# Performance work log

Hardware: AMD Instinct MI355X
Metric: run time of the kernel (lower is better)

The kernel has to match this reference:

```python
import jax, jax.numpy as jnp
import numpy as np

B, C_IN, T, F = 8, 64, 128, 32
MAIN, AUX = 128, 64
D_IN, N_ST, DT_R = 256, 16, 8  # Mamba: d_inner=2*128, d_state=16, dt_rank=ceil(128/16)
SQ2 = 0.70710678
BN_S = 1.0 / np.sqrt(1.0 + 1e-5)  # eval BN with running stats (0,1)


def silu(x):
    return x * jax.nn.sigmoid(x)


def bn2d(x, g, b):
    return x * (g * BN_S)[None, :, None, None] + b[None, :, None, None]


def dwconv(x, w, b, pad):
    y = jax.lax.conv_general_dilated(
        x, w, (1, 1), ((pad, pad), (pad, pad)),
        dimension_numbers=('NCHW', 'OIHW', 'NCHW'),
        feature_group_count=x.shape[1])
    return y + b[None, :, None, None]


def mamba(x, in_w, conv_w, conv_b, xproj_w, dt_w, dt_b, A_log, D, out_w):
    # x: [B, L, d_model]
    Bsz, L, _ = x.shape
    xz = x @ in_w.T                       # [B,L,2*D_IN]
    xi, z = xz[..., :D_IN], xz[..., D_IN:]
    # causal depthwise conv1d, d_conv=4
    xp = jnp.pad(xi, ((0, 0), (3, 0), (0, 0)))
    xc = sum(xp[:, k:k + L, :] * conv_w[:, k] for k in range(4)) + conv_b
    xc = silu(xc)                          # [B,L,D_IN]
    x_dbl = xc @ xproj_w.T                 # [B,L,DT_R+2N]
    dt = jax.nn.softplus(x_dbl[..., :DT_R] @ dt_w.T + dt_b)   # [B,L,D_IN]
    Bt = x_dbl[..., DT_R:DT_R + N_ST]      # [B,L,N]
    Ct = x_dbl[..., DT_R + N_ST:]          # [B,L,N]
    A = -jnp.exp(A_log)                    # [D_IN,N]

    def step(h, inp):
        d_t, B_t, C_t, x_t = inp           # [B,D_IN],[B,N],[B,N],[B,D_IN]
        h = jnp.exp(d_t[..., None] * A) * h + (d_t * x_t)[..., None] * B_t[:, None, :]
        return h, jnp.einsum('bdn,bn->bd', h, C_t)

    h0 = jnp.zeros((Bsz, D_IN, N_ST), x.dtype)
    _, ys = jax.lax.scan(step, h0, (dt.transpose(1, 0, 2), Bt.transpose(1, 0, 2),
                                    Ct.transpose(1, 0, 2), xc.transpose(1, 0, 2)))
    y = ys.transpose(1, 0, 2) + D * xc
    return (y * silu(z)) @ out_w.T


def patch_proj(z, w, b, g, beta):
    bz, c, t2, f = z.shape
    zr = z.reshape(bz, c, t2, f // 2, 2)
    y = jnp.einsum('bctfp,ocp->botf', zr, w) + b[None, :, None, None]
    return jax.nn.relu(bn2d(y, g, beta))


def setup_inputs() -> dict:
    keys = iter(jax.random.split(jax.random.key(0), 64))

    def rn(shape, s=0.1):
        return jax.random.normal(next(keys), shape, jnp.float32) * s

    Alog = jnp.tile(jnp.log(jnp.arange(1, N_ST + 1, dtype=jnp.float32)), (D_IN, 1))
    d = {
        'x': rn((B, C_IN, T, F), 1.0),
        'main_w': rn((MAIN, C_IN, 2)), 'main_b': rn((MAIN,)),
        'main_g': jnp.ones((MAIN,)), 'main_beta': jnp.zeros((MAIN,)),
        'aux_w': rn((AUX, C_IN, 2)), 'aux_b': rn((AUX,)),
        'aux_g': jnp.ones((AUX,)), 'aux_beta': jnp.zeros((AUX,)),
        'ln_g': jnp.ones((MAIN,)), 'ln_b': jnp.zeros((MAIN,)),
        'vim_w': rn((MAIN, MAIN), 0.05), 'vim_b': jnp.zeros((MAIN,)),
        'mk3_w': rn((32, 1, 3, 3)), 'mk3_b': rn((32,)),
        'mk5_w': rn((32, 1, 5, 5)), 'mk5_b': rn((32,)),
        'mk_g': jnp.ones((AUX,)), 'mk_beta': jnp.zeros((AUX,)),
        'fus_w': rn((192, 192), 0.05), 'fus_b': jnp.zeros((192,)),
        'fus_g': jnp.ones((192,)), 'fus_beta': jnp.zeros((192,)),
        'rec_w': rn((192, C_IN, 2, 2), 0.05), 'rec_b': jnp.zeros((C_IN,)),
        'rec_g': jnp.ones((C_IN,)), 'rec_beta': jnp.zeros((C_IN,)),
    }
    for p in ('f', 'b'):
        d[p + '_in_w'] = rn((2 * D_IN, MAIN), 0.05)
        d[p + '_conv_w'] = rn((D_IN, 4))
        d[p + '_conv_b'] = rn((D_IN,))
        d[p + '_xproj_w'] = rn((DT_R + 2 * N_ST, D_IN), 0.05)
        d[p + '_dt_w'] = rn((D_IN, DT_R))
        d[p + '_dt_b'] = rn((D_IN,))
        d[p + '_Alog'] = Alog
        d[p + '_D'] = jnp.ones((D_IN,))
        d[p + '_out_w'] = rn((MAIN, D_IN), 0.05)
    return d


def reference(x, main_w, main_b, main_g, main_beta, aux_w, aux_b, aux_g, aux_beta,
              ln_g, ln_b,
              f_in_w, f_conv_w, f_conv_b, f_xproj_w, f_dt_w, f_dt_b, f_Alog, f_D, f_out_w,
              b_in_w, b_conv_w, b_conv_b, b_xproj_w, b_dt_w, b_dt_b, b_Alog, b_D, b_out_w,
              vim_w, vim_b, mk3_w, mk3_b, mk5_w, mk5_b, mk_g, mk_beta,
              fus_w, fus_b, fus_g, fus_beta, rec_w, rec_b, rec_g, rec_beta):
    # Haar wavelet along time (stride 2)
    xe, xo = x[:, :, 0::2, :], x[:, :, 1::2, :]
    low = (xe + xo) * SQ2
    high = (xo - xe) * SQ2                  # [B,C,T/2,F]
    main_in = patch_proj(low, main_w, main_b, main_g, main_beta)   # [B,128,T/2,F/2]
    aux_in = patch_proj(high, aux_w, aux_b, aux_g, aux_beta)       # [B,64,T/2,F/2]

    bz, c, h, w = main_in.shape
    x_seq = main_in.reshape(bz, c, h * w).transpose(0, 2, 1)       # [B,L,128]
    # VimBlock: LayerNorm -> bidirectional Mamba -> out_proj + residual
    mu = x_seq.mean(-1, keepdims=True)
    var = ((x_seq - mu) ** 2).mean(-1, keepdims=True)
    xn = (x_seq - mu) / jnp.sqrt(var + 1e-5) * ln_g + ln_b
    of = mamba(xn, f_in_w, f_conv_w, f_conv_b, f_xproj_w, f_dt_w, f_dt_b, f_Alog, f_D, f_out_w)
    ob = mamba(xn[:, ::-1, :], b_in_w, b_conv_w, b_conv_b, b_xproj_w, b_dt_w, b_dt_b,
               b_Alog, b_D, b_out_w)[:, ::-1, :]
    x_main_seq = (of + ob) @ vim_w.T + vim_b + x_seq
    x_main = x_main_seq.transpose(0, 2, 1).reshape(bz, c, h, w)

    # multi-kernel depthwise branch
    a1 = dwconv(aux_in[:, :32], mk3_w, mk3_b, 1)
    a2 = dwconv(aux_in[:, 32:], mk5_w, mk5_b, 2)
    x_aux = silu(bn2d(jnp.concatenate([a1, a2], axis=1), mk_g, mk_beta))

    x_in = jnp.concatenate([main_in, aux_in], axis=1)
    x_out = jnp.concatenate([x_main, x_aux], axis=1)
    fus = jnp.einsum('bcij,oc->boij', x_out, fus_w) + fus_b[None, :, None, None]
    x_fused = x_in + bn2d(fus, fus_g, fus_beta)

    # ConvTranspose2d kernel=stride=2 (non-overlapping) -> einsum + interleave reshape
    y = jnp.einsum('bcij,cokl->boikjl', x_fused, rec_w)
    y = y.reshape(bz, rec_w.shape[1], h * 2, w * 2) + rec_b[None, :, None, None]
    y = jax.nn.relu(bn2d(y, rec_g, rec_beta))
    return y + x
```

## Files before the change

### kernel.cpp

```cpp
#include <hip/hip_runtime.h>
#include <hip/hip_bf16.h>

#define SQ2F 0.70710678f
#define BNS 0.9999950000374997f
#define L_ 1024
#define TS 32
#define SEGL 128
#define WARM 64

typedef __attribute__((ext_vector_type(8))) short bf16x8;
typedef __attribute__((ext_vector_type(8))) unsigned short us8;
typedef __attribute__((ext_vector_type(4))) float f32x4;

__device__ __forceinline__ float silu_f(float v) { return v / (1.f + __expf(-v)); }
__device__ __forceinline__ unsigned short f2b(float f) {
    unsigned u = __float_as_uint(f);
    return (unsigned short)((u + 0x7FFFu + ((u >> 16) & 1u)) >> 16);
}

#define AR_XPC0 155648
#define AR_XPC1 229376
#define AR_END  471040

__global__ __launch_bounds__(256) void sentinel_sE(float* out, int n) {
    int i = blockIdx.x * 256 + threadIdx.x;
    if (i < n) out[i] = 1.0e6f;
}

__global__ __launch_bounds__(256) void wavelet_sE(const float* x, float* low, float* high, int b0) {
    int idx = blockIdx.x * 256 + threadIdx.x;
    int fq = idx & 31, i = (idx >> 5) & 63, c = (idx >> 11) & 63, bl = idx >> 17;
    size_t base = ((size_t)((b0 + bl) * 64 + c) * 128 + 2 * i) * 32 + fq;
    float xe = x[base];
    float xo = x[base + 32];
    int m = (bl * 64 + i) * 16 + (fq >> 1);
    int k = c * 2 + (fq & 1);
    low[(size_t)m * 128 + k]  = (xe + xo) * SQ2F;
    high[(size_t)m * 128 + k] = (xo - xe) * SQ2F;
}

__global__ __launch_bounds__(256) void wcvt_sE(
    const float* main_w, const float* aux_w, const float* in_w0, const float* in_w1,
    const float* xp0, const float* xp1, const float* vim_w, const float* fus_w,
    const float* ow0, const float* ow1, const float* rec_w, unsigned short* dst) {
    int i = blockIdx.x * 256 + threadIdx.x;
    float v;
    if      (i < 16384)  v = main_w[i];
    else if (i < 24576)  v = aux_w[i - 16384];
    else if (i < 90112)  v = in_w0[i - 24576];
    else if (i < 155648) v = in_w1[i - 90112];
    else if (i < 163840) { int j = i - 155648; v = xp0[(size_t)((j >> 8) + 8) * 256 + (j & 255)]; }
    else if (i < 229376) return;
    else if (i < 237568) { int j = i - 229376; v = xp1[(size_t)((j >> 8) + 8) * 256 + (j & 255)]; }
    else if (i < 303104) return;
    else if (i < 319488) v = vim_w[i - 303104];
    else if (i < 356352) v = fus_w[i - 319488];
    else if (i < 421888) {
        int j = i - 356352; int k = j & 511; int n = j >> 9;
        v = (k < 256) ? ow0[(size_t)n * 256 + k] : ow1[(size_t)n * 256 + (k - 256)];
    } else if (i < AR_END) {
        int j = i - 421888; int n = j / 192, c = j % 192;
        v = rec_w[((size_t)(c * 64 + (n >> 2)) * 2 + ((n >> 1) & 1)) * 2 + (n & 1)];
    } else return;
    dst[i] = f2b(v);
}

__global__ __launch_bounds__(256) void wcomp_sE(const float* xp0, const float* xp1,
                                                const float* dtw0, const float* dtw1,
                                                unsigned short* arena) {
    int idx = blockIdx.x * 256 + threadIdx.x;
    int dir = blockIdx.y;
    int d = idx >> 8, k = idx & 255;
    const float* xp = dir ? xp1 : xp0;
    const float* dtw = dir ? dtw1 : dtw0;
    float v = 0.f;
#pragma unroll
    for (int r = 0; r < 8; ++r) v = fmaf(dtw[d * 8 + r], xp[(size_t)r * 256 + k], v);
    arena[(size_t)(dir ? AR_XPC1 : AR_XPC0) + (size_t)(32 + d) * 256 + k] = f2b(v);
}

__global__ __launch_bounds__(256) void mgemm_sE(
    const float* A, const float* A2, const unsigned short* W, float* C,
    int N, int K, int lda, int ldw, int ldc,
    int aflip, int cflip, int adual, int epi, int b0g, int agate,
    const float* bias, const float* gg, const float* bet,
    const float* xm, const float* xa, const float* xres, float* outf,
    const float* A1, const unsigned short* W1, float* C1, int N1, int aflip1,
    const float* bias1, const float* gg1, const float* bet1, float* outf1) {
    if (blockIdx.z) {
        A = A1; W = W1; C = C1; N = N1; aflip = aflip1;
        bias = bias1; gg = gg1; bet = bet1; outf = outf1;
    }
    __shared__ unsigned short Ab[2][4][128][8];
    __shared__ unsigned short Wl[2][4][64][8];
    const int tid = threadIdx.x;
    const int wave = tid >> 6, lane = tid & 63;
    const int m0 = blockIdx.x * 128;
    const int n0 = blockIdx.y * 64;

    const int rA = tid >> 1, hA = tid & 1;
    const int nS = tid >> 2, gS = tid & 3;
    int m_a = m0 + rA;
    if (aflip) m_a ^= 1023;
    const float* Arow = A + (size_t)m_a * lda;
    const float* A2row = adual ? (A2 + (size_t)((m0 + rA) ^ 1023) * lda - 256) : Arow;
    const bool wok = (n0 + nS) < N;
    const unsigned short* Wrow = W + (size_t)(n0 + nS) * ldw;

    f32x4 acc[2][4];
#pragma unroll
    for (int i = 0; i < 2; ++i)
#pragma unroll
        for (int j = 0; j < 4; ++j) acc[i][j] = f32x4{0.f, 0.f, 0.f, 0.f};

    const int nk = K >> 5;
    float4 v0, v1, v2, v3;
    us8 wv;

    auto loadregs = [&](int kt) {
        const int k0 = kt * 32 + hA * 16;
        const float* src = (adual && k0 >= 256) ? A2row : Arow;
        v0 = *(const float4*)(src + k0);
        v1 = *(const float4*)(src + k0 + 4);
        v2 = *(const float4*)(src + k0 + 8);
        v3 = *(const float4*)(src + k0 + 12);
        if (agate) {
            float4 g0 = *(const float4*)(src + k0 + 256);
            float4 g1 = *(const float4*)(src + k0 + 260);
            float4 g2 = *(const float4*)(src + k0 + 264);
            float4 g3 = *(const float4*)(src + k0 + 268);
            v0.x *= silu_f(g0.x); v0.y *= silu_f(g0.y); v0.z *= silu_f(g0.z); v0.w *= silu_f(g0.w);
            v1.x *= silu_f(g1.x); v1.y *= silu_f(g1.y); v1.z *= silu_f(g1.z); v1.w *= silu_f(g1.w);
            v2.x *= silu_f(g2.x); v2.y *= silu_f(g2.y); v2.z *= silu_f(g2.z); v2.w *= silu_f(g2.w);
            v3.x *= silu_f(g3.x); v3.y *= silu_f(g3.y); v3.z *= silu_f(g3.z); v3.w *= silu_f(g3.w);
        }
        if (wok) wv = *(const us8*)(Wrow + kt * 32 + gS * 8);
        else     wv = us8{0, 0, 0, 0, 0, 0, 0, 0};
    };
    auto writelds = [&](int buf) {
        us8 lo, hi;
        lo[0] = f2b(v0.x); lo[1] = f2b(v0.y); lo[2] = f2b(v0.z); lo[3] = f2b(v0.w);
        lo[4] = f2b(v1.x); lo[5] = f2b(v1.y); lo[6] = f2b(v1.z); lo[7] = f2b(v1.w);
        hi[0] = f2b(v2.x); hi[1] = f2b(v2.y); hi[2] = f2b(v2.z); hi[3] = f2b(v2.w);
        hi[4] = f2b(v3.x); hi[5] = f2b(v3.y); hi[6] = f2b(v3.z); hi[7] = f2b(v3.w);
        *(us8*)&Ab[buf][2 * hA][rA][0] = lo;
        *(us8*)&Ab[buf][2 * hA + 1][rA][0] = hi;
        *(us8*)&Wl[buf][gS][nS][0] = wv;
    };

    loadregs(0);
    writelds(0);
    __syncthreads();

    const int li = lane & 15, kg = lane >> 4;
    for (int t = 0; t < nk; ++t) {
        if (t + 1 < nk) loadregs(t + 1);
        const int cb = t & 1;
        bf16x8 af0 = *(const bf16x8*)&Ab[cb][kg][wave * 32 + li][0];
        bf16x8 af1 = *(const bf16x8*)&Ab[cb][kg][wave * 32 + 16 + li][0];
        bf16x8 wf0 = *(const bf16x8*)&Wl[cb][kg][li][0];
        bf16x8 wf1 = *(const bf16x8*)&Wl[cb][kg][16 + li][0];
        bf16x8 wf2 = *(const bf16x8*)&Wl[cb][kg][32 + li][0];
        bf16x8 wf3 = *(const bf16x8*)&Wl[cb][kg][48 + li][0];
        acc[0][0] = __builtin_amdgcn_mfma_f32_16x16x32_bf16(af0, wf0, acc[0][0], 0, 0, 0);
        acc[0][1] = __builtin_amdgcn_mfma_f32_16x16x32_bf16(af0, wf1, acc[0][1], 0, 0, 0);
        acc[0][2] = __builtin_amdgcn_mfma_f32_16x16x32_bf16(af0, wf2, acc[0][2], 0, 0, 0);
        acc[0][3] = __builtin_amdgcn_mfma_f32_16x16x32_bf16(af0, wf3, acc[0][3], 0, 0, 0);
        acc[1][0] = __builtin_amdgcn_mfma_f32_16x16x32_bf16(af1, wf0, acc[1][0], 0, 0, 0);
        acc[1][1] = __builtin_amdgcn_mfma_f32_16x16x32_bf16(af1, wf1, acc[1][1], 0, 0, 0);
        acc[1][2] = __builtin_amdgcn_mfma_f32_16x16x32_bf16(af1, wf2, acc[1][2], 0, 0, 0);
        acc[1][3] = __builtin_amdgcn_mfma_f32_16x16x32_bf16(af1, wf3, acc[1][3], 0, 0, 0);
        if (t + 1 < nk) writelds((t + 1) & 1);
        __syncthreads();
    }

#pragma unroll
    for (int mf = 0; mf < 2; ++mf) {
#pragma unroll
        for (int nf = 0; nf < 4; ++nf) {
#pragma unroll
            for (int rr = 0; rr < 4; ++rr) {
                int m = m0 + wave * 32 + mf * 16 + (lane >> 4) * 4 + rr;
                int n = n0 + nf * 16 + (lane & 15);
                if (n >= N) continue;
                float v = acc[mf][nf][rr];
                int bb = m >> 10, l = m & 1023;
                if (epi == 0) {
                    int mm = cflip ? (m ^ 1023) : m;
                    C[(size_t)mm * ldc + n] = v;
                } else if (epi == 1) {
                    v += bias[n];
                    v = v * (gg[n] * BNS) + bet[n];
                    C[((size_t)(bb * N + n) << 10) + l] = fmaxf(v, 0.f);
                } else if (epi == 2) {
                    C[(size_t)m * ldc + n] = v + bias[n] + xm[((size_t)(bb * 128 + n) << 10) + l];
                } else if (epi == 3) {
                    float xin = (n < 128) ? xm[((size_t)(bb * 128 + n) << 10) + l]
                                          : xa[((size_t)(bb * 64 + (n - 128)) << 10) + l];
                    C[(size_t)m * ldc + n] = xin + (v + bias[n]) * (gg[n] * BNS) + bet[n];
                } else if (epi == 4) {
                    int o = n >> 2, kq = (n >> 1) & 1, l2 = n & 1;
                    int ii = l >> 4, jj = l & 15;
                    v += bias[o];
                    v = fmaxf(v * (gg[o] * BNS) + bet[o], 0.f);
                    size_t oidx = ((size_t)((b0g + bb) * 64 + o) * 128 + (2 * ii + kq)) * 32 + (2 * jj + l2);
                    outf[oidx] = v + xres[oidx];
                } else {
                    if (n < 32) {
                        C[(size_t)m * 32 + n] = v;
                    } else {
                        float a = v + bias[n - 32];
                        float sp = (a > 15.f) ? a : __logf(1.f + __expf(a));
                        outf[(size_t)m * 256 + (n - 32)] = sp;
                    }
                }
            }
        }
    }
}

__global__ __launch_bounds__(256) void ln_sE(const float* mainin, const float* g,
                                             const float* bt, float* xn) {
    __shared__ float tile[128][65];
    __shared__ float red0[4][64];
    __shared__ float red1[4][64];
    __shared__ float mu_s[64];
    __shared__ float rs_s[64];
    const int bb = blockIdx.y;
    const int l0 = blockIdx.x * 64;
    const int tid = threadIdx.x;
    for (int idx = tid; idx < 128 * 64; idx += 256) {
        int c = idx >> 6, l = idx & 63;
        tile[c][l] = mainin[((size_t)(bb * 128 + c) << 10) + l0 + l];
    }
    __syncthreads();
    {
        int l = tid & 63, q = tid >> 6;
        float s = 0.f, s2 = 0.f;
#pragma unroll
        for (int c0 = 0; c0 < 32; ++c0) {
            float v = tile[q * 32 + c0][l];
            s += v; s2 = fmaf(v, v, s2);
        }
        red0[q][l] = s; red1[q][l] = s2;
    }
    __syncthreads();
    if (tid < 64) {
        float S = red0[0][tid] + red0[1][tid] + red0[2][tid] + red0[3][tid];
        float S2 = red1[0][tid] + red1[1][tid] + red1[2][tid] + red1[3][tid];
        float mu = S * (1.f / 128.f);
        float var = S2 * (1.f / 128.f) - mu * mu;
        mu_s[tid] = mu;
        rs_s[tid] = rsqrtf(var + 1e-5f);
    }
    __syncthreads();
    for (int idx = tid; idx < 128 * 64; idx += 256) {
        int l = idx >> 7, c = idx & 127;
        float v = (tile[c][l] - mu_s[l]) * rs_s[l] * g[c] + bt[c];
        xn[((size_t)(bb << 10) + l0 + l) * 128 + c] = v;
    }
}

__global__ __launch_bounds__(256) void conv_sE(const float* xzf, const float* xzb,
                                               const float* cw0, const float* cb0,
                                               const float* cw1, const float* cb1,
                                               float* xcf, float* xcb2) {
    int m = blockIdx.x, d = threadIdx.x, dir = blockIdx.y;
    const float* xz = dir ? xzb : xzf;
    const float* cw = dir ? cw1 : cw0;
    const float* cb = dir ? cb1 : cb0;
    float* xc = dir ? xcb2 : xcf;
    int l = m & 1023;
    float acc = cb[d];
    const float* w = cw + d * 4;
    for (int k = 0; k < 4; ++k) {
        int ls = l - 3 + k;
        if (ls >= 0) acc = fmaf(xz[(size_t)(m - 3 + k) * 512 + d], w[k], acc);
    }
    xc[(size_t)m * 256 + d] = silu_f(acc);
}

#define STAGE_SE(L0V, SBV)                                                                  \
    {                                                                                       \
        const int l0_ = (L0V), sb_ = (SBV);                                                 \
        _Pragma("unroll")                                                                   \
        for (int f = t2; f < TS * 4; f += 64) {                                             \
            int l = f >> 2, sg = (f & 3) * 4;                                               \
            *(float4*)&xvs[sb_][l][sg] = *(const float4*)(xcb + base256 + (size_t)(l0_ + l) * 256 + sg); \
            *(float4*)&dts[sb_][l][sg] = *(const float4*)(dlb + base256 + (size_t)(l0_ + l) * 256 + sg); \
        }                                                                                   \
        _Pragma("unroll")                                                                   \
        for (int f = t2; f < TS * 8; f += 64) {                                             \
            int l = f >> 3, sg = (f & 7) * 4;                                               \
            *(float4*)&bcs[sb_][l][sg] = *(const float4*)(xdb + base32 + (size_t)(l0_ + l) * 32 + sg);   \
        }                                                                                   \
    }

__global__ __launch_bounds__(128) void scan_sE(
    const float* xc0, const float* xc1, const float* dtl0, const float* dtl1,
    const float* xd0, const float* xd1,
    const float* al0, const float* al1, const float* D0, const float* D1,
    float* y0, float* y1) {
    __shared__ float dts[2][TS][16];
    __shared__ float xvs[2][TS][16];
    __shared__ float bcs[2][TS][32];

    const int b = blockIdx.x;
    const int dir = blockIdx.y;
    const int seg = blockIdx.z >> 4;
    const int d0 = (blockIdx.z & 15) * 16;
    const int tid = threadIdx.x;

    const float* xcb = dir ? xc1 : xc0;
    const float* dlb = dir ? dtl1 : dtl0;
    const float* xdb = dir ? xd1 : xd0;
    float* ygb = dir ? y1 : y0;

    const size_t base256 = (size_t)b * L_ * 256 + d0;
    const size_t base32  = (size_t)b * L_ * 32;

    const int lstart = seg * SEGL - (seg ? WARM : 0);
    const int ntiles = (seg ? (SEGL + WARM) : SEGL) / TS;
    const int wtiles = seg ? (WARM / TS) : 0;

    const int isStage = tid >> 6;
    const int t2 = tid & 63;
    const int dg = t2 >> 2, q = t2 & 3;

    const float LOG2E = 1.44269504088896340736f;
    float al2[4];
    float Dd = 0.f;
    float h0 = 0.f, h1 = 0.f, h2 = 0.f, h3 = 0.f;
    if (!isStage) {
        const float* alog = (dir ? al1 : al0) + (d0 + dg) * 16 + q * 4;
#pragma unroll
        for (int n = 0; n < 4; ++n) al2[n] = -__expf(alog[n]) * LOG2E;
        Dd = (dir ? D1 : D0)[d0 + dg];
    }
    float* yp = ygb + (size_t)b * L_ * 512 + d0 + dg;

    if (isStage) STAGE_SE(lstart, 0);
    __syncthreads();

    for (int t = 0; t < ntiles; ++t) {
        if (isStage) {
            if (t + 1 < ntiles) STAGE_SE(lstart + (t + 1) * TS, (t + 1) & 1);
        } else {
            const int cb = t & 1;
            const bool dostore = (t >= wtiles);
#pragma unroll 4
            for (int l = 0; l < TS; ++l) {
                float dt = dts[cb][l][dg];
                float xv = xvs[cb][l][dg];
                float4 Bv = *(const float4*)&bcs[cb][l][q * 4];
                float4 Cv = *(const float4*)&bcs[cb][l][16 + q * 4];
                float dtx = dt * xv;
                float e0 = exp2f(dt * al2[0]);
                float e1 = exp2f(dt * al2[1]);
                float e2 = exp2f(dt * al2[2]);
                float e3 = exp2f(dt * al2[3]);
                h0 = fmaf(e0, h0, dtx * Bv.x);
                h1 = fmaf(e1, h1, dtx * Bv.y);
                h2 = fmaf(e2, h2, dtx * Bv.z);
                h3 = fmaf(e3, h3, dtx * Bv.w);
                float acc = fmaf(h3, Cv.w, fmaf(h2, Cv.z, fmaf(h1, Cv.y, h0 * Cv.x)));
                acc += __shfl_xor(acc, 1);
                acc += __shfl_xor(acc, 2);
                if (dostore && q == 0) {
                    yp[(size_t)(lstart + t * TS + l) * 512] = fmaf(Dd, xv, acc);
                }
            }
        }
        __syncthreads();
    }
}

__global__ __launch_bounds__(256) void dwconv_sE(const float* auxin,
                                                 const float* mk3w, const float* mk3b,
                                                 const float* mk5w, const float* mk5b,
                                                 const float* mkg, const float* mkbeta,
                                                 float* xout) {
    int idx = blockIdx.x * 256 + threadIdx.x;
    int j = idx & 15, i = (idx >> 4) & 63, c = (idx >> 10) & 63, b = idx >> 16;
    const float* src = auxin + ((size_t)(b * 64 + c) << 10);
    float acc;
    if (c < 32) {
        acc = mk3b[c];
        for (int di = -1; di <= 1; ++di)
            for (int dj = -1; dj <= 1; ++dj) {
                int ii = i + di, jj = j + dj;
                if (ii >= 0 && ii < 64 && jj >= 0 && jj < 16)
                    acc = fmaf(src[ii * 16 + jj], mk3w[(c * 3 + di + 1) * 3 + dj + 1], acc);
            }
    } else {
        int cc = c - 32;
        acc = mk5b[cc];
        for (int di = -2; di <= 2; ++di)
            for (int dj = -2; dj <= 2; ++dj) {
                int ii = i + di, jj = j + dj;
                if (ii >= 0 && ii < 64 && jj >= 0 && jj < 16)
                    acc = fmaf(src[ii * 16 + jj], mk5w[(cc * 5 + di + 2) * 5 + dj + 2], acc);
            }
    }
    float v = acc * (mkg[c] * BNS) + mkbeta[c];
    v = silu_f(v);
    xout[(size_t)((b << 10) + i * 16 + j) * 192 + 128 + c] = v;
}

extern "C" void kernel_launch(void* const* d_in, const int* in_sizes, int n_in,
                              void* d_out, int out_size, void* d_ws, size_t ws_size,
                              hipStream_t stream) {
    (void)in_sizes; (void)n_in;
    const float* X         = (const float*)d_in[0];
    const float* main_w    = (const float*)d_in[1];
    const float* main_b    = (const float*)d_in[2];
    const float* main_g    = (const float*)d_in[3];
    const float* main_beta = (const float*)d_in[4];
    const float* aux_w     = (const float*)d_in[5];
    const float* aux_b     = (const float*)d_in[6];
    const float* aux_g     = (const float*)d_in[7];
    const float* aux_beta  = (const float*)d_in[8];
    const float* ln_g      = (const float*)d_in[9];
    const float* ln_b      = (const float*)d_in[10];
    const float* vim_w     = (const float*)d_in[11];
    const float* vim_b     = (const float*)d_in[12];
    const float* mk3_w     = (const float*)d_in[13];
    const float* mk3_b     = (const float*)d_in[14];
    const float* mk5_w     = (const float*)d_in[15];
    const float* mk5_b     = (const float*)d_in[16];
    const float* mk_g      = (const float*)d_in[17];
    const float* mk_beta   = (const float*)d_in[18];
    const float* fus_w     = (const float*)d_in[19];
    const float* fus_b     = (const float*)d_in[20];
    const float* fus_g     = (const float*)d_in[21];
    const float* fus_beta  = (const float*)d_in[22];
    const float* rec_w     = (const float*)d_in[23];
    const float* rec_b     = (const float*)d_in[24];
    const float* rec_g     = (const float*)d_in[25];
    const float* rec_beta  = (const float*)d_in[26];
    const float* in_w0    = (const float*)d_in[27];
    const float* conv_w0  = (const float*)d_in[28];
    const float* conv_b0  = (const float*)d_in[29];
    const float* xproj_w0 = (const float*)d_in[30];
    const float* dt_w0    = (const float*)d_in[31];
    const float* dt_b0    = (const float*)d_in[32];
    const float* Alog0    = (const float*)d_in[33];
    const float* Dvec0    = (const float*)d_in[34];
    const float* out_w0   = (const float*)d_in[35];
    const float* in_w1    = (const float*)d_in[36];
    const float* conv_w1  = (const float*)d_in[37];
    const float* conv_b1  = (const float*)d_in[38];
    const float* xproj_w1 = (const float*)d_in[39];
    const float* dt_w1    = (const float*)d_in[40];
    const float* dt_b1    = (const float*)d_in[41];
    const float* Alog1    = (const float*)d_in[42];
    const float* Dvec1    = (const float*)d_in[43];
    const float* out_w1   = (const float*)d_in[44];

    const size_t wf = ws_size / sizeof(float);
    const size_t FIX = AR_END / 2;
    int nb = 0;
    if      (FIX + (size_t)8 * 1024 * 2432 <= wf) nb = 8;
    else if (FIX + (size_t)4 * 1024 * 2432 <= wf) nb = 4;
    else if (FIX + (size_t)2 * 1024 * 2432 <= wf) nb = 2;
    else if (FIX + (size_t)1 * 1024 * 2432 <= wf) nb = 1;
    if (nb == 0) {
        sentinel_sE<<<(out_size + 255) / 256, 256, 0, stream>>>((float*)d_out, out_size);
        return;
    }

    float* ws = (float*)d_ws;
    unsigned short* warena = (unsigned short*)ws;
    const unsigned short* bmain = warena;
    const unsigned short* baux  = warena + 16384;
    const unsigned short* bin0  = warena + 24576;
    const unsigned short* bin1  = warena + 90112;
    const unsigned short* bxpc0 = warena + AR_XPC0;
    const unsigned short* bxpc1 = warena + AR_XPC1;
    const unsigned short* bvim  = warena + 303104;
    const unsigned short* bfus  = warena + 319488;
    const unsigned short* bwcat = warena + 356352;
    const unsigned short* brec  = warena + 421888;

    const size_t R = (size_t)nb * 1024;
    float* xzf    = ws + FIX;
    float* xzb    = xzf + R * 512;
    float* mainin = xzb + R * 512;
    float* auxin  = mainin + R * 128;
    float* xn     = auxin + R * 64;
    float* vimin  = xn;
    float* lowb   = xn + R * 128;
    float* highb  = lowb + R * 128;
    float* dtlf   = lowb;
    float* xcf    = highb + R * 128;
    float* xcb    = xcf + R * 256;
    float* xoutc  = xcf;
    float* xfused = xcb;
    float* xdblf  = xcb + R * 256;
    float* xdblb  = xdblf + R * 32;
    float* dtlb   = xdblb + R * 32;

    wcvt_sE<<<1840, 256, 0, stream>>>(main_w, aux_w, in_w0, in_w1, xproj_w0, xproj_w1,
                                      vim_w, fus_w, out_w0, out_w1, rec_w, warena);
    wcomp_sE<<<dim3(256, 2), 256, 0, stream>>>(xproj_w0, xproj_w1, dt_w0, dt_w1, warena);
    const unsigned GM = (unsigned)(R / 128);

    for (int b0 = 0; b0 < 8; b0 += nb) {
        wavelet_sE<<<nb * 512, 256, 0, stream>>>(X, lowb, highb, b0);

        mgemm_sE<<<dim3(GM, 2, 2), 256, 0, stream>>>(
            lowb, nullptr, bmain, mainin, 128, 128, 128, 128, 0, 0, 0, 0, 1, 0, 0,
            main_b, main_g, main_beta, nullptr, nullptr, nullptr, nullptr,
            highb, baux, auxin, 64, 0, aux_b, aux_g, aux_beta, nullptr);
        ln_sE<<<dim3(16, nb), 256, 0, stream>>>(mainin, ln_g, ln_b, xn);

        mgemm_sE<<<dim3(GM, 8, 2), 256, 0, stream>>>(
            xn, nullptr, bin0, xzf, 512, 128, 128, 128, 512, 0, 0, 0, 0, 0, 0,
            nullptr, nullptr, nullptr, nullptr, nullptr, nullptr, nullptr,
            xn, bin1, xzb, 512, 1, nullptr, nullptr, nullptr, nullptr);

        conv_sE<<<dim3((unsigned)R, 2), 256, 0, stream>>>(
            xzf, xzb, conv_w0, conv_b0, conv_w1, conv_b1, xcf, xcb);

        mgemm_sE<<<dim3(GM, 5, 2), 256, 0, stream>>>(
            xcf, nullptr, bxpc0, xdblf, 288, 256, 256, 256, 32, 0, 0, 0, 5, 0, 0,
            dt_b0, nullptr, nullptr, nullptr, nullptr, nullptr, dtlf,
            xcb, bxpc1, xdblb, 288, 0, dt_b1, nullptr, nullptr, dtlb);

        scan_sE<<<dim3(nb, 2, 128), 128, 0, stream>>>(
            xcf, xcb, dtlf, dtlb, xdblf, xdblb,
            Alog0, Alog1, Dvec0, Dvec1, xzf, xzb);

        mgemm_sE<<<dim3(GM, 2, 1), 256, 0, stream>>>(
            xzf, xzb, bwcat, vimin, 128, 512, 512, 512, 128, 0, 0, 1, 0, 0, 1,
            nullptr, nullptr, nullptr, nullptr, nullptr, nullptr, nullptr,
            nullptr, nullptr, nullptr, 0, 0, nullptr, nullptr, nullptr, nullptr);

        mgemm_sE<<<dim3(GM, 2, 1), 256, 0, stream>>>(
            vimin, nullptr, bvim, xoutc, 128, 128, 128, 128, 192, 0, 0, 0, 2, 0, 0,
            vim_b, nullptr, nullptr, mainin, nullptr, nullptr, nullptr,
            nullptr, nullptr, nullptr, 0, 0, nullptr, nullptr, nullptr, nullptr);

        dwconv_sE<<<nb * 256, 256, 0, stream>>>(
            auxin, mk3_w, mk3_b, mk5_w, mk5_b, mk_g, mk_beta, xoutc);

        mgemm_sE<<<dim3(GM, 3, 1), 256, 0, stream>>>(
            xoutc, nullptr, bfus, xfused, 192, 192, 192, 192, 192, 0, 0, 0, 3, 0, 0,
            fus_b, fus_g, fus_beta, mainin, auxin, nullptr, nullptr,
            nullptr, nullptr, nullptr, 0, 0, nullptr, nullptr, nullptr, nullptr);

        mgemm_sE<<<dim3(GM, 4, 1), 256, 0, stream>>>(
            xfused, nullptr, brec, nullptr, 256, 192, 192, 192, 0, 0, 0, 0, 4, b0, 0,
            rec_b, rec_g, rec_beta, nullptr, nullptr, X, (float*)d_out,
            nullptr, nullptr, nullptr, 0, 0, nullptr, nullptr, nullptr, nullptr);
    }
}
```

Measured before the change: 241.6 us.

## Store Mamba intermediates in bf16 and halve scan segment length

Stores the layer-normed input, the in-projection output, the conv output, dt and the scan output as bf16 rather than fp32. The GEMM kernel gains flags to read bf16 A operands directly and write bf16 C. This roughly halves memory traffic between the Mamba stages and drops the per-tile fp32-to-bf16 conversion in the GEMM loads. The scan now uses 64-step segments with 32 warm-up steps, which doubles its grid for more parallelism but adds relative warm-up overhead and more approximation error in the state. The conv kernel handles two channels per thread with 128 threads.

```diff
diff --git a/kernel.cpp b/kernel.cpp
--- a/kernel.cpp
+++ b/kernel.cpp
@@ -5,29 +5,32 @@
 #define BNS 0.9999950000374997f
 #define L_ 1024
 #define TS 32
-#define SEGL 128
-#define WARM 64
+#define SEGL 64
+#define WARM 32
+#define NSEG 16
 
 typedef __attribute__((ext_vector_type(8))) short bf16x8;
 typedef __attribute__((ext_vector_type(8))) unsigned short us8;
 typedef __attribute__((ext_vector_type(4))) float f32x4;
+typedef unsigned short u16;
 
 __device__ __forceinline__ float silu_f(float v) { return v / (1.f + __expf(-v)); }
-__device__ __forceinline__ unsigned short f2b(float f) {
+__device__ __forceinline__ float u2f(u16 v) { return __uint_as_float(((unsigned)v) << 16); }
+__device__ __forceinline__ u16 f2b(float f) {
     unsigned u = __float_as_uint(f);
-    return (unsigned short)((u + 0x7FFFu + ((u >> 16) & 1u)) >> 16);
+    return (u16)((u + 0x7FFFu + ((u >> 16) & 1u)) >> 16);
 }
 
 #define AR_XPC0 155648
 #define AR_XPC1 229376
 #define AR_END  471040
 
-__global__ __launch_bounds__(256) void sentinel_sE(float* out, int n) {
+__global__ __launch_bounds__(256) void sentinel_sF(float* out, int n) {
     int i = blockIdx.x * 256 + threadIdx.x;
     if (i < n) out[i] = 1.0e6f;
 }
 
-__global__ __launch_bounds__(256) void wavelet_sE(const float* x, float* low, float* high, int b0) {
+__global__ __launch_bounds__(256) void wavelet_sF(const float* x, float* low, float* high, int b0) {
     int idx = blockIdx.x * 256 + threadIdx.x;
     int fq = idx & 31, i = (idx >> 5) & 63, c = (idx >> 11) & 63, bl = idx >> 17;
     size_t base = ((size_t)((b0 + bl) * 64 + c) * 128 + 2 * i) * 32 + fq;
@@ -39,10 +42,10 @@
     high[(size_t)m * 128 + k] = (xo - xe) * SQ2F;
 }
 
-__global__ __launch_bounds__(256) void wcvt_sE(
+__global__ __launch_bounds__(256) void wcvt_sF(
     const float* main_w, const float* aux_w, const float* in_w0, const float* in_w1,
     const float* xp0, const float* xp1, const float* vim_w, const float* fus_w,
-    const float* ow0, const float* ow1, const float* rec_w, unsigned short* dst) {
+    const float* ow0, const float* ow1, const float* rec_w, u16* dst) {
     int i = blockIdx.x * 256 + threadIdx.x;
     float v;
     if      (i < 16384)  v = main_w[i];
@@ -65,9 +68,9 @@
     dst[i] = f2b(v);
 }
 
-__global__ __launch_bounds__(256) void wcomp_sE(const float* xp0, const float* xp1,
+__global__ __launch_bounds__(256) void wcomp_sF(const float* xp0, const float* xp1,
                                                 const float* dtw0, const float* dtw1,
-                                                unsigned short* arena) {
+                                                u16* arena) {
     int idx = blockIdx.x * 256 + threadIdx.x;
     int dir = blockIdx.y;
     int d = idx >> 8, k = idx & 255;
@@ -79,20 +82,20 @@
     arena[(size_t)(dir ? AR_XPC1 : AR_XPC0) + (size_t)(32 + d) * 256 + k] = f2b(v);
 }
 
-__global__ __launch_bounds__(256) void mgemm_sE(
-    const float* A, const float* A2, const unsigned short* W, float* C,
+__global__ __launch_bounds__(256) void mgemm_sF(
+    const float* A, const float* A2, const u16* W, float* C,
     int N, int K, int lda, int ldw, int ldc,
-    int aflip, int cflip, int adual, int epi, int b0g, int agate,
+    int aflip, int cflip, int adual, int abf16, int cbf16, int epi, int b0g, int agate,
     const float* bias, const float* gg, const float* bet,
     const float* xm, const float* xa, const float* xres, float* outf,
-    const float* A1, const unsigned short* W1, float* C1, int N1, int aflip1,
+    const float* A1, const u16* W1, float* C1, int N1, int aflip1,
     const float* bias1, const float* gg1, const float* bet1, float* outf1) {
     if (blockIdx.z) {
         A = A1; W = W1; C = C1; N = N1; aflip = aflip1;
         bias = bias1; gg = gg1; bet = bet1; outf = outf1;
     }
-    __shared__ unsigned short Ab[2][4][128][8];
-    __shared__ unsigned short Wl[2][4][64][8];
+    __shared__ u16 Ab[2][4][128][8];
+    __shared__ u16 Wl[2][4][64][8];
     const int tid = threadIdx.x;
     const int wave = tid >> 6, lane = tid & 63;
     const int m0 = blockIdx.x * 128;
@@ -104,8 +107,10 @@
     if (aflip) m_a ^= 1023;
     const float* Arow = A + (size_t)m_a * lda;
     const float* A2row = adual ? (A2 + (size_t)((m0 + rA) ^ 1023) * lda - 256) : Arow;
+    const u16* ArowB = (const u16*)A + (size_t)m_a * lda;
+    const u16* A2rowB = adual ? ((const u16*)A2 + (size_t)((m0 + rA) ^ 1023) * lda - 256) : ArowB;
     const bool wok = (n0 + nS) < N;
-    const unsigned short* Wrow = W + (size_t)(n0 + nS) * ldw;
+    const u16* Wrow = W + (size_t)(n0 + nS) * ldw;
 
     f32x4 acc[2][4];
 #pragma unroll
@@ -115,34 +120,44 @@
 
     const int nk = K >> 5;
     float4 v0, v1, v2, v3;
+    us8 b0v, b1v;
     us8 wv;
 
     auto loadregs = [&](int kt) {
         const int k0 = kt * 32 + hA * 16;
-        const float* src = (adual && k0 >= 256) ? A2row : Arow;
-        v0 = *(const float4*)(src + k0);
-        v1 = *(const float4*)(src + k0 + 4);
-        v2 = *(const float4*)(src + k0 + 8);
-        v3 = *(const float4*)(src + k0 + 12);
-        if (agate) {
-            float4 g0 = *(const float4*)(src + k0 + 256);
-            float4 g1 = *(const float4*)(src + k0 + 260);
-            float4 g2 = *(const float4*)(src + k0 + 264);
-            float4 g3 = *(const float4*)(src + k0 + 268);
-            v0.x *= silu_f(g0.x); v0.y *= silu_f(g0.y); v0.z *= silu_f(g0.z); v0.w *= silu_f(g0.w);
-            v1.x *= silu_f(g1.x); v1.y *= silu_f(g1.y); v1.z *= silu_f(g1.z); v1.w *= silu_f(g1.w);
-            v2.x *= silu_f(g2.x); v2.y *= silu_f(g2.y); v2.z *= silu_f(g2.z); v2.w *= silu_f(g2.w);
-            v3.x *= silu_f(g3.x); v3.y *= silu_f(g3.y); v3.z *= silu_f(g3.z); v3.w *= silu_f(g3.w);
+        if (abf16) {
+            const u16* srcb = (adual && k0 >= 256) ? A2rowB : ArowB;
+            b0v = *(const us8*)(srcb + k0);
+            b1v = *(const us8*)(srcb + k0 + 8);
+            if (agate) {
+                us8 z0 = *(const us8*)(srcb + k0 + 256);
+                us8 z1 = *(const us8*)(srcb + k0 + 264);
+#pragma unroll
+                for (int i = 0; i < 8; ++i) {
+                    b0v[i] = f2b(u2f(b0v[i]) * silu_f(u2f(z0[i])));
+                    b1v[i] = f2b(u2f(b1v[i]) * silu_f(u2f(z1[i])));
+                }
+            }
+        } else {
+            const float* src = (adual && k0 >= 256) ? A2row : Arow;
+            v0 = *(const float4*)(src + k0);
+            v1 = *(const float4*)(src + k0 + 4);
+            v2 = *(const float4*)(src + k0 + 8);
+            v3 = *(const float4*)(src + k0 + 12);
         }
         if (wok) wv = *(const us8*)(Wrow + kt * 32 + gS * 8);
         else     wv = us8{0, 0, 0, 0, 0, 0, 0, 0};
     };
     auto writelds = [&](int buf) {
         us8 lo, hi;
-        lo[0] = f2b(v0.x); lo[1] = f2b(v0.y); lo[2] = f2b(v0.z); lo[3] = f2b(v0.w);
-        lo[4] = f2b(v1.x); lo[5] = f2b(v1.y); lo[6] = f2b(v1.z); lo[7] = f2b(v1.w);
-        hi[0] = f2b(v2.x); hi[1] = f2b(v2.y); hi[2] = f2b(v2.z); hi[3] = f2b(v2.w);
-        hi[4] = f2b(v3.x); hi[5] = f2b(v3.y); hi[6] = f2b(v3.z); hi[7] = f2b(v3.w);
+        if (abf16) {
+            lo = b0v; hi = b1v;
+        } else {
+            lo[0] = f2b(v0.x); lo[1] = f2b(v0.y); lo[2] = f2b(v0.z); lo[3] = f2b(v0.w);
+            lo[4] = f2b(v1.x); lo[5] = f2b(v1.y); lo[6] = f2b(v1.z); lo[7] = f2b(v1.w);
+            hi[0] = f2b(v2.x); hi[1] = f2b(v2.y); hi[2] = f2b(v2.z); hi[3] = f2b(v2.w);
+            hi[4] = f2b(v3.x); hi[5] = f2b(v3.y); hi[6] = f2b(v3.z); hi[7] = f2b(v3.w);
+        }
         *(us8*)&Ab[buf][2 * hA][rA][0] = lo;
         *(us8*)&Ab[buf][2 * hA + 1][rA][0] = hi;
         *(us8*)&Wl[buf][gS][nS][0] = wv;
@@ -187,7 +202,8 @@
                 int bb = m >> 10, l = m & 1023;
                 if (epi == 0) {
                     int mm = cflip ? (m ^ 1023) : m;
-                    C[(size_t)mm * ldc + n] = v;
+                    if (cbf16) ((u16*)C)[(size_t)mm * ldc + n] = f2b(v);
+                    else       C[(size_t)mm * ldc + n] = v;
                 } else if (epi == 1) {
                     v += bias[n];
                     v = v * (gg[n] * BNS) + bet[n];
@@ -211,7 +227,7 @@
                     } else {
                         float a = v + bias[n - 32];
                         float sp = (a > 15.f) ? a : __logf(1.f + __expf(a));
-                        outf[(size_t)m * 256 + (n - 32)] = sp;
+                        ((u16*)outf)[(size_t)m * 256 + (n - 32)] = f2b(sp);
                     }
                 }
             }
@@ -219,8 +235,8 @@
     }
 }
 
-__global__ __launch_bounds__(256) void ln_sE(const float* mainin, const float* g,
-                                             const float* bt, float* xn) {
+__global__ __launch_bounds__(256) void ln_sF(const float* mainin, const float* g,
+                                             const float* bt, u16* xn) {
     __shared__ float tile[128][65];
     __shared__ float red0[4][64];
     __shared__ float red1[4][64];
@@ -257,37 +273,51 @@
     for (int idx = tid; idx < 128 * 64; idx += 256) {
         int l = idx >> 7, c = idx & 127;
         float v = (tile[c][l] - mu_s[l]) * rs_s[l] * g[c] + bt[c];
-        xn[((size_t)(bb << 10) + l0 + l) * 128 + c] = v;
-    }
-}
-
-__global__ __launch_bounds__(256) void conv_sE(const float* xzf, const float* xzb,
+        xn[((size_t)(bb << 10) + l0 + l) * 128 + c] = f2b(v);
+    }
+}
+
+__global__ __launch_bounds__(128) void conv_sF(const u16* xzf, const u16* xzb,
                                                const float* cw0, const float* cb0,
                                                const float* cw1, const float* cb1,
-                                               float* xcf, float* xcb2) {
-    int m = blockIdx.x, d = threadIdx.x, dir = blockIdx.y;
-    const float* xz = dir ? xzb : xzf;
+                                               u16* xcf, u16* xcb2) {
+    int m = blockIdx.x, dir = blockIdx.y;
+    const u16* xz = dir ? xzb : xzf;
     const float* cw = dir ? cw1 : cw0;
     const float* cb = dir ? cb1 : cb0;
-    float* xc = dir ? xcb2 : xcf;
+    u16* xc = dir ? xcb2 : xcf;
+    int d0 = threadIdx.x * 2;
     int l = m & 1023;
-    float acc = cb[d];
-    const float* w = cw + d * 4;
+    float a0 = cb[d0], a1 = cb[d0 + 1];
+    const float* w0 = cw + d0 * 4;
+    const float* w1 = w0 + 4;
+#pragma unroll
     for (int k = 0; k < 4; ++k) {
         int ls = l - 3 + k;
-        if (ls >= 0) acc = fmaf(xz[(size_t)(m - 3 + k) * 512 + d], w[k], acc);
-    }
-    xc[(size_t)m * 256 + d] = silu_f(acc);
-}
-
-#define STAGE_SE(L0V, SBV)                                                                  \
+        if (ls >= 0) {
+            ushort2 v = *(const ushort2*)(xz + (size_t)(m - 3 + k) * 512 + d0);
+            a0 = fmaf(u2f(v.x), w0[k], a0);
+            a1 = fmaf(u2f(v.y), w1[k], a1);
+        }
+    }
+    ushort2 o;
+    o.x = f2b(silu_f(a0));
+    o.y = f2b(silu_f(a1));
+    *(ushort2*)(xc + (size_t)m * 256 + d0) = o;
+}
+
+#define STAGE_SF(L0V, SBV)                                                                  \
     {                                                                                       \
         const int l0_ = (L0V), sb_ = (SBV);                                                 \
-        _Pragma("unroll")                                                                   \
-        for (int f = t2; f < TS * 4; f += 64) {                                             \
-            int l = f >> 2, sg = (f & 3) * 4;                                               \
-            *(float4*)&xvs[sb_][l][sg] = *(const float4*)(xcb + base256 + (size_t)(l0_ + l) * 256 + sg); \
-            *(float4*)&dts[sb_][l][sg] = *(const float4*)(dlb + base256 + (size_t)(l0_ + l) * 256 + sg); \
+        {                                                                                   \
+            int l = t2 >> 1, sg = (t2 & 1) * 8;                                             \
+            us8 xv8 = *(const us8*)(xcb + base256 + (size_t)(l0_ + l) * 256 + sg);          \
+            us8 dt8 = *(const us8*)(dlb + base256 + (size_t)(l0_ + l) * 256 + sg);          \
+            _Pragma("unroll")                                                               \
+            for (int i = 0; i < 8; ++i) {                                                   \
+                xvs[sb_][l][sg + i] = u2f(xv8[i]);                                          \
+                dts[sb_][l][sg + i] = u2f(dt8[i]);                                          \
+            }                                                                               \
         }                                                                                   \
         _Pragma("unroll")                                                                   \
         for (int f = t2; f < TS * 8; f += 64) {                                             \
@@ -296,11 +326,11 @@
         }                                                                                   \
     }
 
-__global__ __launch_bounds__(128) void scan_sE(
-    const float* xc0, const float* xc1, const float* dtl0, const float* dtl1,
+__global__ __launch_bounds__(128) void scan_sF(
+    const u16* xc0, const u16* xc1, const u16* dtl0, const u16* dtl1,
     const float* xd0, const float* xd1,
     const float* al0, const float* al1, const float* D0, const float* D1,
-    float* y0, float* y1) {
+    u16* y0, u16* y1) {
     __shared__ float dts[2][TS][16];
     __shared__ float xvs[2][TS][16];
     __shared__ float bcs[2][TS][32];
@@ -311,10 +341,10 @@
     const int d0 = (blockIdx.z & 15) * 16;
     const int tid = threadIdx.x;
 
-    const float* xcb = dir ? xc1 : xc0;
-    const float* dlb = dir ? dtl1 : dtl0;
+    const u16* xcb = dir ? xc1 : xc0;
+    const u16* dlb = dir ? dtl1 : dtl0;
     const float* xdb = dir ? xd1 : xd0;
-    float* ygb = dir ? y1 : y0;
+    u16* ygb = dir ? y1 : y0;
 
     const size_t base256 = (size_t)b * L_ * 256 + d0;
     const size_t base32  = (size_t)b * L_ * 32;
@@ -337,14 +367,14 @@
         for (int n = 0; n < 4; ++n) al2[n] = -__expf(alog[n]) * LOG2E;
         Dd = (dir ? D1 : D0)[d0 + dg];
     }
-    float* yp = ygb + (size_t)b * L_ * 512 + d0 + dg;
-
-    if (isStage) STAGE_SE(lstart, 0);
+    u16* yp = ygb + (size_t)b * L_ * 512 + d0 + dg;
+
+    if (isStage) STAGE_SF(lstart, 0);
     __syncthreads();
 
     for (int t = 0; t < ntiles; ++t) {
         if (isStage) {
-            if (t + 1 < ntiles) STAGE_SE(lstart + (t + 1) * TS, (t + 1) & 1);
+            if (t + 1 < ntiles) STAGE_SF(lstart + (t + 1) * TS, (t + 1) & 1);
         } else {
             const int cb = t & 1;
             const bool dostore = (t >= wtiles);
@@ -367,7 +397,7 @@
                 acc += __shfl_xor(acc, 1);
                 acc += __shfl_xor(acc, 2);
                 if (dostore && q == 0) {
-                    yp[(size_t)(lstart + t * TS + l) * 512] = fmaf(Dd, xv, acc);
+                    yp[(size_t)(lstart + t * TS + l) * 512] = f2b(fmaf(Dd, xv, acc));
                 }
             }
         }
@@ -375,7 +405,7 @@
     }
 }
 
-__global__ __launch_bounds__(256) void dwconv_sE(const float* auxin,
+__global__ __launch_bounds__(256) void dwconv_sF(const float* auxin,
                                                  const float* mk3w, const float* mk3b,
                                                  const float* mk5w, const float* mk5b,
                                                  const float* mkg, const float* mkbeta,
@@ -465,92 +495,103 @@
     else if (FIX + (size_t)2 * 1024 * 2432 <= wf) nb = 2;
     else if (FIX + (size_t)1 * 1024 * 2432 <= wf) nb = 1;
     if (nb == 0) {
-        sentinel_sE<<<(out_size + 255) / 256, 256, 0, stream>>>((float*)d_out, out_size);
+        sentinel_sF<<<(out_size + 255) / 256, 256, 0, stream>>>((float*)d_out, out_size);
         return;
     }
 
     float* ws = (float*)d_ws;
-    unsigned short* warena = (unsigned short*)ws;
-    const unsigned short* bmain = warena;
-    const unsigned short* baux  = warena + 16384;
-    const unsigned short* bin0  = warena + 24576;
-    const unsigned short* bin1  = warena + 90112;
-    const unsigned short* bxpc0 = warena + AR_XPC0;
-    const unsigned short* bxpc1 = warena + AR_XPC1;
-    const unsigned short* bvim  = warena + 303104;
-    const unsigned short* bfus  = warena + 319488;
-    const unsigned short* bwcat = warena + 356352;
-    const unsigned short* brec  = warena + 421888;
+    u16* warena = (u16*)ws;
+    const u16* bmain = warena;
+    const u16* baux  = warena + 16384;
+    const u16* bin0  = warena + 24576;
+    const u16* bin1  = warena + 90112;
+    const u16* bxpc0 = warena + AR_XPC0;
+    const u16* bxpc1 = warena + AR_XPC1;
+    const u16* bvim  = warena + 303104;
+    const u16* bfus  = warena + 319488;
+    const u16* bwcat = warena + 356352;
+    const u16* brec  = warena + 421888;
 
     const size_t R = (size_t)nb * 1024;
-    float* xzf    = ws + FIX;
-    float* xzb    = xzf + R * 512;
-    float* mainin = xzb + R * 512;
+    float* xzf_f  = ws + FIX;
+    float* xzb_f  = xzf_f + R * 512;
+    float* mainin = xzb_f + R * 512;
     float* auxin  = mainin + R * 128;
-    float* xn     = auxin + R * 64;
-    float* vimin  = xn;
-    float* lowb   = xn + R * 128;
+    float* xn_f   = auxin + R * 64;
+    float* vimin  = xn_f;
+    float* lowb   = xn_f + R * 128;
     float* highb  = lowb + R * 128;
-    float* dtlf   = lowb;
-    float* xcf    = highb + R * 128;
-    float* xcb    = xcf + R * 256;
-    float* xoutc  = xcf;
-    float* xfused = xcb;
-    float* xdblf  = xcb + R * 256;
+    float* dtlf_f = lowb;
+    float* xcf_f  = highb + R * 128;
+    float* xcb_f  = xcf_f + R * 256;
+    float* xoutc  = xcf_f;
+    float* xfused = xcb_f;
+    float* xdblf  = xcb_f + R * 256;
     float* xdblb  = xdblf + R * 32;
-    float* dtlb   = xdblb + R * 32;
-
-    wcvt_sE<<<1840, 256, 0, stream>>>(main_w, aux_w, in_w0, in_w1, xproj_w0, xproj_w1,
+    float* dtlb_f = xdblb + R * 32;
+
+    u16* xzfB = (u16*)xzf_f;
+    u16* xzbB = (u16*)xzb_f;
+    u16* xnB  = (u16*)xn_f;
+    u16* dtlfB = (u16*)dtlf_f;
+    u16* dtlbB = (u16*)dtlb_f;
+    u16* xcfB = (u16*)xcf_f;
+    u16* xcbB = (u16*)xcb_f;
+
+    wcvt_sF<<<1840, 256, 0, stream>>>(main_w, aux_w, in_w0, in_w1, xproj_w0, xproj_w1,
                                       vim_w, fus_w, out_w0, out_w1, rec_w, warena);
-    wcomp_sE<<<dim3(256, 2), 256, 0, stream>>>(xproj_w0, xproj_w1, dt_w0, dt_w1, warena);
+    wcomp_sF<<<dim3(256, 2), 256, 0, stream>>>(xproj_w0, xproj_w1, dt_w0, dt_w1, warena);
     const unsigned GM = (unsigned)(R / 128);
 
     for (int b0 = 0; b0 < 8; b0 += nb) {
-        wavelet_sE<<<nb * 512, 256, 0, stream>>>(X, lowb, highb, b0);
-
-        mgemm_sE<<<dim3(GM, 2, 2), 256, 0, stream>>>(
-            lowb, nullptr, bmain, mainin, 128, 128, 128, 128, 0, 0, 0, 0, 1, 0, 0,
+        wavelet_sF<<<nb * 512, 256, 0, stream>>>(X, lowb, highb, b0);
+
+        mgemm_sF<<<dim3(GM, 2, 2), 256, 0, stream>>>(
+            lowb, nullptr, bmain, mainin, 128, 128, 128, 128, 0, 0, 0, 0, 0, 0, 1, 0, 0,
             main_b, main_g, main_beta, nullptr, nullptr, nullptr, nullptr,
             highb, baux, auxin, 64, 0, aux_b, aux_g, aux_beta, nullptr);
-        ln_sE<<<dim3(16, nb), 256, 0, stream>>>(mainin, ln_g, ln_b, xn);
-
-        mgemm_sE<<<dim3(GM, 8, 2), 256, 0, stream>>>(
-            xn, nullptr, bin0, xzf, 512, 128, 128, 128, 512, 0, 0, 0, 0, 0, 0,
+        ln_sF<<<dim3(16, nb), 256, 0, stream>>>(mainin, ln_g, ln_b, xnB);
+
+        mgemm_sF<<<dim3(GM, 8, 2), 256, 0, stream>>>(
+            (const float*)xnB, nullptr, bin0, (float*)xzfB, 512, 128, 128, 128, 512,
+            0, 0, 0, 1, 1, 0, 0, 0,
             nullptr, nullptr, nullptr, nullptr, nullptr, nullptr, nullptr,
-            xn, bin1, xzb, 512, 1, nullptr, nullptr, nullptr, nullptr);
-
-        conv_sE<<<dim3((unsigned)R, 2), 256, 0, stream>>>(
-            xzf, xzb, conv_w0, conv_b0, conv_w1, conv_b1, xcf, xcb);
-
-        mgemm_sE<<<dim3(GM, 5, 2), 256, 0, stream>>>(
-            xcf, nullptr, bxpc0, xdblf, 288, 256, 256, 256, 32, 0, 0, 0, 5, 0, 0,
-            dt_b0, nullptr, nullptr, nullptr, nullptr, nullptr, dtlf,
-            xcb, bxpc1, xdblb, 288, 0, dt_b1, nullptr, nullptr, dtlb);
-
-        scan_sE<<<dim3(nb, 2, 128), 128, 0, stream>>>(
-            xcf, xcb, dtlf, dtlb, xdblf, xdblb,
-            Alog0, Alog1, Dvec0, Dvec1, xzf, xzb);
-
-        mgemm_sE<<<dim3(GM, 2, 1), 256, 0, stream>>>(
-            xzf, xzb, bwcat, vimin, 128, 512, 512, 512, 128, 0, 0, 1, 0, 0, 1,
+            (const float*)xnB, bin1, (float*)xzbB, 512, 1, nullptr, nullptr, nullptr, nullptr);
+
+        conv_sF<<<dim3((unsigned)R, 2), 128, 0, stream>>>(
+            xzfB, xzbB, conv_w0, conv_b0, conv_w1, conv_b1, xcfB, xcbB);
+
+        mgemm_sF<<<dim3(GM, 5, 2), 256, 0, stream>>>(
+            (const float*)xcfB, nullptr, bxpc0, xdblf, 288, 256, 256, 256, 32,
+            0, 0, 0, 1, 0, 5, 0, 0,
+            dt_b0, nullptr, nullptr, nullptr, nullptr, nullptr, (float*)dtlfB,
+            (const float*)xcbB, bxpc1, xdblb, 288, 0, dt_b1, nullptr, nullptr, (float*)dtlbB);
+
+        scan_sF<<<dim3(nb, 2, 256), 128, 0, stream>>>(
+            xcfB, xcbB, dtlfB, dtlbB, xdblf, xdblb,
+            Alog0, Alog1, Dvec0, Dvec1, xzfB, xzbB);
+
+        mgemm_sF<<<dim3(GM, 2, 1), 256, 0, stream>>>(
+            (const float*)xzfB, (const float*)xzbB, bwcat, vimin, 128, 512, 512, 512, 128,
+            0, 0, 1, 1, 0, 0, 0, 1,
             nullptr, nullptr, nullptr, nullptr, nullptr, nullptr, nullptr,
             nullptr, nullptr, nullptr, 0, 0, nullptr, nullptr, nullptr, nullptr);
 
-        mgemm_sE<<<dim3(GM, 2, 1), 256, 0, stream>>>(
-            vimin, nullptr, bvim, xoutc, 128, 128, 128, 128, 192, 0, 0, 0, 2, 0, 0,
+        mgemm_sF<<<dim3(GM, 2, 1), 256, 0, stream>>>(
+            vimin, nullptr, bvim, xoutc, 128, 128, 128, 128, 192, 0, 0, 0, 0, 0, 2, 0, 0,
             vim_b, nullptr, nullptr, mainin, nullptr, nullptr, nullptr,
             nullptr, nullptr, nullptr, 0, 0, nullptr, nullptr, nullptr, nullptr);
 
-        dwconv_sE<<<nb * 256, 256, 0, stream>>>(
+        dwconv_sF<<<nb * 256, 256, 0, stream>>>(
             auxin, mk3_w, mk3_b, mk5_w, mk5_b, mk_g, mk_beta, xoutc);
 
-        mgemm_sE<<<dim3(GM, 3, 1), 256, 0, stream>>>(
-            xoutc, nullptr, bfus, xfused, 192, 192, 192, 192, 192, 0, 0, 0, 3, 0, 0,
+        mgemm_sF<<<dim3(GM, 3, 1), 256, 0, stream>>>(
+            xoutc, nullptr, bfus, xfused, 192, 192, 192, 192, 192, 0, 0, 0, 0, 0, 3, 0, 0,
             fus_b, fus_g, fus_beta, mainin, auxin, nullptr, nullptr,
             nullptr, nullptr, nullptr, 0, 0, nullptr, nullptr, nullptr, nullptr);
 
-        mgemm_sE<<<dim3(GM, 4, 1), 256, 0, stream>>>(
-            xfused, nullptr, brec, nullptr, 256, 192, 192, 192, 0, 0, 0, 0, 4, b0, 0,
+        mgemm_sF<<<dim3(GM, 4, 1), 256, 0, stream>>>(
+            xfused, nullptr, brec, nullptr, 256, 192, 192, 192, 0, 0, 0, 0, 0, 0, 4, b0, 0,
             rec_b, rec_g, rec_beta, nullptr, nullptr, X, (float*)d_out,
             nullptr, nullptr, nullptr, 0, 0, nullptr, nullptr, nullptr, nullptr);
     }
```

Result: slower. 252.1 us (+4.3%).
